# Kernel optimization log

Measured on AMD Instinct MI355X. Metric: run time of the kernel, lower is better.

The kernel has to match this reference:

```python
import jax, jax.numpy as jnp
import numpy as np

NUM_HEADS = 6
WS = 3

def setup_inputs() -> dict:
    key = jax.random.key(0)
    k1, k2, k3 = jax.random.split(key, 3)
    dim = 192
    x = jax.random.normal(k1, (2, dim, 48, 48, 48), dtype=jnp.float32)
    Wqkv = jax.random.normal(k2, (3 * dim, dim), dtype=jnp.float32) * (dim ** -0.5)
    Wproj = jax.random.normal(k3, (dim, dim), dtype=jnp.float32) * (dim ** -0.5)
    bproj = jnp.zeros((dim,), dtype=jnp.float32)
    return {"x": x, "Wqkv": Wqkv, "Wproj": Wproj, "bproj": bproj, "H": 384, "W": 288}

def reference(x, Wqkv, Wproj, bproj, H, W):
    b, c, h, w, d = x.shape
    xt = x.reshape(b, -1, c)                      # (B, N, C) with C = c, N = h*w*d
    B, N, C = xt.shape
    nh, ws = NUM_HEADS, WS
    hd = C // nh
    scale = hd ** -0.5
    hg, wg = H // ws, W // ws
    tg = hg * wg
    # window partition: (B, hg, ws, wg, ws, C) -> (B, hg, wg, ws, ws, C)
    xw = xt.reshape(B, hg, ws, wg, ws, C).transpose(0, 1, 3, 2, 4, 5)
    # fused QKV projection (no bias)
    qkv = jnp.einsum('bgvijc,oc->bgvijo', xw, Wqkv)          # (B,hg,wg,ws,ws,3C)
    qkv = qkv.reshape(B, tg, ws * ws, 3, nh, hd).transpose(3, 0, 1, 4, 2, 5)
    q, k, v = qkv[0], qkv[1], qkv[2]                          # (B, tg, nh, 9, hd)
    attn = jnp.einsum('bgnqd,bgnkd->bgnqk', q, k) * scale     # (B, tg, nh, 9, 9)
    attn = jax.nn.softmax(attn, axis=-1)
    out = jnp.einsum('bgnqk,bgnkd->bgnqd', attn, v)           # (B, tg, nh, 9, hd)
    out = out.transpose(0, 1, 3, 2, 4).reshape(B, hg, wg, ws, ws, C)
    out = jnp.swapaxes(out, 2, 3).reshape(B, N, C)            # un-window
    out = out @ Wproj.T + bproj
    return out.reshape(b, c, h, w, d)
```

## Files before the change

### kernel.cpp

```cpp
#include <hip/hip_runtime.h>

typedef _Float16 f16;
typedef _Float16 f16x4 __attribute__((ext_vector_type(4)));
typedef _Float16 f16x8 __attribute__((ext_vector_type(8)));
typedef float f32x4 __attribute__((ext_vector_type(4)));

#define TPB  576
#define NWIN 16
#define XS   200
#define WSS  200
#define QS   40
#define VS   260
#define VSF  264

#define WSQF_HALVES 110592
#define WS_NEEDED   (221184 + 73728)

__global__ __launch_bounds__(512) void conv_w(
    const float* __restrict__ Wqkv, const float* __restrict__ Wproj,
    f16* __restrict__ wsWqf, f16* __restrict__ wsWpf)
{
    int idx = blockIdx.x * 512 + threadIdx.x;
    if (idx < WSQF_HALVES) {
        int h    = idx / 18432;
        int rem  = idx % 18432;
        int ct   = rem / 3072;
        int rem2 = rem % 3072;
        int kk   = rem2 / 512;
        int rem3 = rem2 % 512;
        int lane = rem3 / 8;
        int e    = rem3 % 8;
        int r    = 16 * ct + (lane & 15);
        int grow = (r >> 5) * 192 + h * 32 + (r & 31);
        int col  = kk * 32 + (lane >> 4) * 8 + e;
        wsWqf[idx] = (f16)Wqkv[grow * 192 + col];
    } else {
        int j    = idx - WSQF_HALVES;
        int h    = j / 6144;
        int rem  = j % 6144;
        int nt   = rem / 512;
        int rem2 = rem % 512;
        int lane = rem2 / 8;
        int e    = rem2 % 8;
        wsWpf[j] = (f16)Wproj[(16 * nt + (lane & 15)) * 192 + h * 32 + (lane >> 4) * 8 + e];
    }
}

__global__ __launch_bounds__(TPB) void lsa_mfma12(
    const float* __restrict__ x, const f16* __restrict__ wsWqf,
    const f16* __restrict__ wsWpf, const float* __restrict__ bproj,
    float* __restrict__ out)
{
    __shared__ __attribute__((aligned(16))) f16 Xh[144 * XS];
    __shared__ __attribute__((aligned(16))) f16 Qh2[2][144 * QS];
    __shared__ __attribute__((aligned(16))) f16 Kh2[2][144 * QS];
    __shared__ __attribute__((aligned(16))) f16 Vt2[2][32 * VS];
    __shared__ __attribute__((aligned(16))) f16 AOh2[2][144 * QS];

    const int tid  = threadIdx.x;
    const int lane = tid & 63;
    const int w    = tid >> 6;
    const int ci   = w / 3;
    const int ti   = w % 3;
    const int l15  = lane & 15;
    const int lg   = lane >> 4;

    const int  bb    = blockIdx.x / 768;
    const int  gbase = (blockIdx.x % 768) * NWIN;
    const long rb0   = (long)bb * 110592 + (long)(gbase / 96) * 864 + (long)(gbase % 96) * 3;

    const f16x8* wqf = (const f16x8*)wsWqf;
    const f16x8* wpf = (const f16x8*)wsWpf;

    for (int idx = tid; idx < 144 * 48; idx += TPB) {
        int t = idx / 48, c4 = idx % 48;
        int wi = t / 9, q = t - 9 * wi;
        long grow = rb0 + wi * 3 + (q / 3) * 288 + (q % 3);
        float4 xv = ((const float4*)x)[grow * 48 + c4];
        union { f16 h[4]; ushort4 u; } tmp;
        tmp.h[0] = (f16)xv.x; tmp.h[1] = (f16)xv.y; tmp.h[2] = (f16)xv.z; tmp.h[3] = (f16)xv.w;
        *(ushort4*)&Xh[t * XS + c4 * 4] = tmp.u;
    }
    {
        int4 z = {0, 0, 0, 0};
        for (int i2 = tid; i2 < (2 * 32 * VS * 2) / 16; i2 += TPB) ((int4*)Vt2)[i2] = z;
    }

    f32x4 pacc[3][4];
    #pragma unroll
    for (int a = 0; a < 3; ++a)
        #pragma unroll
        for (int bq = 0; bq < 4; ++bq)
            pacc[a][bq] = (f32x4){0.f, 0.f, 0.f, 0.f};

    __syncthreads();

    for (int p = 0; p < 3; ++p) {
        #pragma unroll
        for (int hh = 0; hh < 2; ++hh) {
            const int h = 2 * p + hh;
            f32x4 qacc[2][3];
            #pragma unroll
            for (int c = 0; c < 2; ++c)
                #pragma unroll
                for (int t = 0; t < 3; ++t)
                    qacc[c][t] = (f32x4){0.f, 0.f, 0.f, 0.f};
            #pragma unroll
            for (int kk = 0; kk < 6; ++kk) {
                f16x8 af[2], bf[3];
                af[0] = wqf[((h * 6 + ci    ) * 6 + kk) * 64 + lane];
                af[1] = wqf[((h * 6 + ci + 3) * 6 + kk) * 64 + lane];
                #pragma unroll
                for (int t = 0; t < 3; ++t)
                    bf[t] = *(const f16x8*)&Xh[(16 * (ti + 3 * t) + l15) * XS + kk * 32 + lg * 8];
                #pragma unroll
                for (int c = 0; c < 2; ++c)
                    #pragma unroll
                    for (int t = 0; t < 3; ++t)
                        qacc[c][t] = __builtin_amdgcn_mfma_f32_16x16x32_f16(af[c], bf[t], qacc[c][t], 0, 0, 0);
            }
            #pragma unroll
            for (int c = 0; c < 2; ++c) {
                const int ct = ci + 3 * c;
                #pragma unroll
                for (int t = 0; t < 3; ++t) {
                    const int token = 16 * (ti + 3 * t) + l15;
                    f16x4 ph;
                    ph[0] = (f16)qacc[c][t][0]; ph[1] = (f16)qacc[c][t][1];
                    ph[2] = (f16)qacc[c][t][2]; ph[3] = (f16)qacc[c][t][3];
                    if (ct < 2) {
                        *(f16x4*)&Qh2[hh][token * QS + ct * 16 + 4 * lg] = ph;
                    } else if (ct < 4) {
                        *(f16x4*)&Kh2[hh][token * QS + (ct - 2) * 16 + 4 * lg] = ph;
                    } else {
                        const int d0 = (ct - 4) * 16 + 4 * lg;
                        int wi = token / 9, qq = token - 9 * wi;
                        #pragma unroll
                        for (int r = 0; r < 4; ++r)
                            Vt2[hh][(d0 + r) * VS + 16 * wi + qq] = ph[r];
                    }
                }
            }
        }
        __syncthreads();

        for (int idx = w; idx < 32; idx += 9) {
            const int hh = idx >> 4;
            const int wi = idx & 15;
            const f16* Qb = &Qh2[hh][0];
            const f16* Kb = &Kh2[hh][0];
            const f16* Vb = &Vt2[hh][0];
            f16* Ab = &AOh2[hh][0];
            int krow = 9 * wi + l15;
            krow = krow > 143 ? 143 : krow;
            f16x8 ak = *(const f16x8*)&Kb[krow * QS + lg * 8];
            f16x8 aq = *(const f16x8*)&Qb[krow * QS + lg * 8];
            f32x4 s = (f32x4){0.f, 0.f, 0.f, 0.f};
            s = __builtin_amdgcn_mfma_f32_16x16x32_f16(ak, aq, s, 0, 0, 0);
            float lgt[4];
            float mx = -1e30f;
            #pragma unroll
            for (int r = 0; r < 4; ++r) {
                int kx = 4 * lg + r;
                lgt[r] = (kx < 9) ? s[r] * 0.17677669529663687f : -1e30f;
                mx = fmaxf(mx, lgt[r]);
            }
            mx = fmaxf(mx, __shfl_xor(mx, 16));
            mx = fmaxf(mx, __shfl_xor(mx, 32));
            float e[4], sum = 0.f;
            #pragma unroll
            for (int r = 0; r < 4; ++r) {
                int kx = 4 * lg + r;
                e[r] = (kx < 9) ? __expf(lgt[r] - mx) : 0.f;
                sum += e[r];
            }
            sum += __shfl_xor(sum, 16);
            sum += __shfl_xor(sum, 32);
            float inv = 1.0f / sum;
            f16x4 pfrag;
            pfrag[0] = (f16)(e[0] * inv); pfrag[1] = (f16)(e[1] * inv);
            pfrag[2] = (f16)(e[2] * inv); pfrag[3] = (f16)(e[3] * inv);
            #pragma unroll
            for (int dt = 0; dt < 2; ++dt) {
                f16x4 av = *(const f16x4*)&Vb[(dt * 16 + l15) * VS + 16 * wi + 4 * lg];
                f32x4 o = (f32x4){0.f, 0.f, 0.f, 0.f};
                o = __builtin_amdgcn_mfma_f32_16x16x16f16(av, pfrag, o, 0, 0, 0);
                if (l15 < 9) {
                    f16x4 oh;
                    oh[0] = (f16)o[0]; oh[1] = (f16)o[1]; oh[2] = (f16)o[2]; oh[3] = (f16)o[3];
                    *(f16x4*)&Ab[(9 * wi + l15) * QS + dt * 16 + 4 * lg] = oh;
                }
            }
        }
        __syncthreads();

        #pragma unroll
        for (int hh = 0; hh < 2; ++hh) {
            const int h = 2 * p + hh;
            f16x8 bw[4];
            #pragma unroll
            for (int bq = 0; bq < 4; ++bq)
                bw[bq] = wpf[(h * 12 + 4 * ti + bq) * 64 + lane];
            f16x8 aof[3];
            #pragma unroll
            for (int a = 0; a < 3; ++a)
                aof[a] = *(const f16x8*)&AOh2[hh][(16 * (3 * ci + a) + l15) * QS + lg * 8];
            #pragma unroll
            for (int bq = 0; bq < 4; ++bq)
                #pragma unroll
                for (int a = 0; a < 3; ++a)
                    pacc[a][bq] = __builtin_amdgcn_mfma_f32_16x16x32_f16(aof[a], bw[bq], pacc[a][bq], 0, 0, 0);
        }
    }

    float bv[4];
    #pragma unroll
    for (int bq = 0; bq < 4; ++bq)
        bv[bq] = bproj[16 * (4 * ti + bq) + l15];
    #pragma unroll
    for (int a = 0; a < 3; ++a) {
        #pragma unroll
        for (int r = 0; r < 4; ++r) {
            int t = 16 * (3 * ci + a) + lg * 4 + r;
            int wi = t / 9, q = t - 9 * wi;
            long grow = rb0 + wi * 3 + (q / 3) * 288 + (q % 3);
            float* dst = out + grow * 192;
            #pragma unroll
            for (int bq = 0; bq < 4; ++bq)
                dst[16 * (4 * ti + bq) + l15] = pacc[a][bq][r] + bv[bq];
        }
    }
}

__global__ __launch_bounds__(TPB) void lsa_mfma7(
    const float* __restrict__ x, const float* __restrict__ Wqkv,
    const float* __restrict__ Wproj, const float* __restrict__ bproj,
    float* __restrict__ out)
{
    __shared__ f16 Xh[144 * XS];
    __shared__ f16 Wh[96 * WSS];
    __shared__ f16 Qh[144 * QS];
    __shared__ f16 Kh[144 * QS];
    __shared__ f16 Vt2f[32 * VSF];
    __shared__ f16 AOh[144 * QS];
    __shared__ f16 Wp[192 * QS];

    const int tid  = threadIdx.x;
    const int lane = tid & 63;
    const int w    = tid >> 6;
    const int ci   = w / 3;
    const int ti   = w % 3;
    const int l15  = lane & 15;
    const int lg   = lane >> 4;

    const int  bb    = blockIdx.x / 768;
    const int  gbase = (blockIdx.x % 768) * NWIN;
    const long rb0   = (long)bb * 110592 + (long)(gbase / 96) * 864 + (long)(gbase % 96) * 3;

    const float4* Wq4 = (const float4*)Wqkv;
    const float4* Wp4 = (const float4*)Wproj;

    for (int idx = tid; idx < 144 * 48; idx += TPB) {
        int t = idx / 48, c4 = idx % 48;
        int wi = t / 9, q = t - 9 * wi;
        long grow = rb0 + wi * 3 + (q / 3) * 288 + (q % 3);
        float4 xv = ((const float4*)x)[grow * 48 + c4];
        union { f16 h[4]; ushort4 u; } tmp;
        tmp.h[0] = (f16)xv.x; tmp.h[1] = (f16)xv.y; tmp.h[2] = (f16)xv.z; tmp.h[3] = (f16)xv.w;
        *(ushort4*)&Xh[t * XS + c4 * 4] = tmp.u;
    }
    {
        int4 z = {0, 0, 0, 0};
        for (int i2 = tid; i2 < (32 * VSF * 2) / 16; i2 += TPB) ((int4*)Vt2f)[i2] = z;
    }
    #pragma unroll
    for (int i = 0; i < 8; ++i) {
        int l = i * TPB + tid;
        int r = l / 48, c4 = l % 48;
        float4 wv = Wq4[((r >> 5) * 192 + (r & 31)) * 48 + c4];
        union { f16 h4[4]; ushort4 u; } t;
        t.h4[0] = (f16)wv.x; t.h4[1] = (f16)wv.y; t.h4[2] = (f16)wv.z; t.h4[3] = (f16)wv.w;
        *(ushort4*)&Wh[r * WSS + c4 * 4] = t.u;
    }

    f32x4 pacc[3][4];
    #pragma unroll
    for (int a = 0; a < 3; ++a)
        #pragma unroll
        for (int bq = 0; bq < 4; ++bq)
            pacc[a][bq] = (f32x4){0.f, 0.f, 0.f, 0.f};

    __syncthreads();

    for (int h = 0; h < 6; ++h) {
        f32x4 qacc[2][3];
        #pragma unroll
        for (int c = 0; c < 2; ++c)
            #pragma unroll
            for (int t = 0; t < 3; ++t)
                qacc[c][t] = (f32x4){0.f, 0.f, 0.f, 0.f};
        #pragma unroll
        for (int kk = 0; kk < 6; ++kk) {
            f16x8 af[2], bf[3];
            #pragma unroll
            for (int c = 0; c < 2; ++c)
                af[c] = *(const f16x8*)&Wh[(16 * (ci + 3 * c) + l15) * WSS + kk * 32 + lg * 8];
            #pragma unroll
            for (int t = 0; t < 3; ++t)
                bf[t] = *(const f16x8*)&Xh[(16 * (ti + 3 * t) + l15) * XS + kk * 32 + lg * 8];
            #pragma unroll
            for (int c = 0; c < 2; ++c)
                #pragma unroll
                for (int t = 0; t < 3; ++t)
                    qacc[c][t] = __builtin_amdgcn_mfma_f32_16x16x32_f16(af[c], bf[t], qacc[c][t], 0, 0, 0);
        }
        #pragma unroll
        for (int c = 0; c < 2; ++c) {
            const int ct = ci + 3 * c;
            #pragma unroll
            for (int t = 0; t < 3; ++t) {
                const int token = 16 * (ti + 3 * t) + l15;
                f16x4 ph;
                ph[0] = (f16)qacc[c][t][0]; ph[1] = (f16)qacc[c][t][1];
                ph[2] = (f16)qacc[c][t][2]; ph[3] = (f16)qacc[c][t][3];
                if (ct < 2) {
                    *(f16x4*)&Qh[token * QS + ct * 16 + 4 * lg] = ph;
                } else if (ct < 4) {
                    *(f16x4*)&Kh[token * QS + (ct - 2) * 16 + 4 * lg] = ph;
                } else {
                    const int d0 = (ct - 4) * 16 + 4 * lg;
                    int wi = token / 9, qq = token - 9 * wi;
                    #pragma unroll
                    for (int r = 0; r < 4; ++r)
                        Vt2f[(d0 + r) * VSF + 16 * wi + qq] = ph[r];
                }
            }
        }
        __syncthreads();

        float4 wpv[3];
        if (tid < 512) {
            #pragma unroll
            for (int i = 0; i < 3; ++i) {
                int l = i * 512 + tid;
                int r = l / 8, c4 = l % 8;
                wpv[i] = Wp4[r * 48 + h * 8 + c4];
            }
        }
        if (h < 5) {
            #pragma unroll
            for (int i = 0; i < 8; ++i) {
                int l = i * TPB + tid;
                int r = l / 48, c4 = l % 48;
                float4 wv = Wq4[((r >> 5) * 192 + (h + 1) * 32 + (r & 31)) * 48 + c4];
                union { f16 h4[4]; ushort4 u; } t;
                t.h4[0] = (f16)wv.x; t.h4[1] = (f16)wv.y; t.h4[2] = (f16)wv.z; t.h4[3] = (f16)wv.w;
                *(ushort4*)&Wh[r * WSS + c4 * 4] = t.u;
            }
        }
        for (int wi = w; wi < NWIN; wi += 9) {
            int krow = 9 * wi + l15;
            krow = krow > 143 ? 143 : krow;
            f16x8 ak = *(const f16x8*)&Kh[krow * QS + lg * 8];
            f16x8 aq = *(const f16x8*)&Qh[krow * QS + lg * 8];
            f32x4 s = (f32x4){0.f, 0.f, 0.f, 0.f};
            s = __builtin_amdgcn_mfma_f32_16x16x32_f16(ak, aq, s, 0, 0, 0);
            float lgt[4];
            float mx = -1e30f;
            #pragma unroll
            for (int r = 0; r < 4; ++r) {
                int kx = 4 * lg + r;
                lgt[r] = (kx < 9) ? s[r] * 0.17677669529663687f : -1e30f;
                mx = fmaxf(mx, lgt[r]);
            }
            mx = fmaxf(mx, __shfl_xor(mx, 16));
            mx = fmaxf(mx, __shfl_xor(mx, 32));
            float e[4], sum = 0.f;
            #pragma unroll
            for (int r = 0; r < 4; ++r) {
                int kx = 4 * lg + r;
                e[r] = (kx < 9) ? __expf(lgt[r] - mx) : 0.f;
                sum += e[r];
            }
            sum += __shfl_xor(sum, 16);
            sum += __shfl_xor(sum, 32);
            float inv = 1.0f / sum;
            f16x4 pf;
            pf[0] = (f16)(e[0] * inv); pf[1] = (f16)(e[1] * inv);
            pf[2] = (f16)(e[2] * inv); pf[3] = (f16)(e[3] * inv);
            #pragma unroll
            for (int dt = 0; dt < 2; ++dt) {
                f16x4 av = *(const f16x4*)&Vt2f[(dt * 16 + l15) * VSF + 16 * wi + 4 * lg];
                f32x4 o = (f32x4){0.f, 0.f, 0.f, 0.f};
                o = __builtin_amdgcn_mfma_f32_16x16x16f16(av, pf, o, 0, 0, 0);
                if (l15 < 9) {
                    f16x4 oh;
                    oh[0] = (f16)o[0]; oh[1] = (f16)o[1]; oh[2] = (f16)o[2]; oh[3] = (f16)o[3];
                    *(f16x4*)&AOh[(9 * wi + l15) * QS + dt * 16 + 4 * lg] = oh;
                }
            }
        }
        if (tid < 512) {
            #pragma unroll
            for (int i = 0; i < 3; ++i) {
                int l = i * 512 + tid;
                int r = l / 8, c4 = l % 8;
                union { f16 h4[4]; ushort4 u; } t;
                t.h4[0] = (f16)wpv[i].x; t.h4[1] = (f16)wpv[i].y;
                t.h4[2] = (f16)wpv[i].z; t.h4[3] = (f16)wpv[i].w;
                *(ushort4*)&Wp[r * QS + c4 * 4] = t.u;
            }
        }
        __syncthreads();

        {
            f16x8 aof[3];
            #pragma unroll
            for (int a = 0; a < 3; ++a)
                aof[a] = *(const f16x8*)&AOh[(16 * (3 * ci + a) + l15) * QS + lg * 8];
            #pragma unroll
            for (int bq = 0; bq < 4; ++bq) {
                f16x8 bw = *(const f16x8*)&Wp[(16 * (4 * ti + bq) + l15) * QS + lg * 8];
                #pragma unroll
                for (int a = 0; a < 3; ++a)
                    pacc[a][bq] = __builtin_amdgcn_mfma_f32_16x16x32_f16(aof[a], bw, pacc[a][bq], 0, 0, 0);
            }
        }
    }

    float bv[4];
    #pragma unroll
    for (int bq = 0; bq < 4; ++bq)
        bv[bq] = bproj[16 * (4 * ti + bq) + l15];
    #pragma unroll
    for (int a = 0; a < 3; ++a) {
        #pragma unroll
        for (int r = 0; r < 4; ++r) {
            int t = 16 * (3 * ci + a) + lg * 4 + r;
            int wi = t / 9, q = t - 9 * wi;
            long grow = rb0 + wi * 3 + (q / 3) * 288 + (q % 3);
            float* dst = out + grow * 192;
            #pragma unroll
            for (int bq = 0; bq < 4; ++bq)
                dst[16 * (4 * ti + bq) + l15] = pacc[a][bq][r] + bv[bq];
        }
    }
}

extern "C" void kernel_launch(void* const* d_in, const int* in_sizes, int n_in,
                              void* d_out, int out_size, void* d_ws, size_t ws_size,
                              hipStream_t stream) {
    const float* x     = (const float*)d_in[0];
    const float* Wqkv  = (const float*)d_in[1];
    const float* Wproj = (const float*)d_in[2];
    const float* bproj = (const float*)d_in[3];
    float* out = (float*)d_out;
    if (ws_size >= (size_t)WS_NEEDED && d_ws != nullptr) {
        f16* wsWqf = (f16*)d_ws;
        f16* wsWpf = (f16*)((char*)d_ws + 221184);
        conv_w<<<288, 512, 0, stream>>>(Wqkv, Wproj, wsWqf, wsWpf);
        lsa_mfma12<<<1536, TPB, 0, stream>>>(x, wsWqf, wsWpf, bproj, out);
    } else {
        lsa_mfma7<<<1536, TPB, 0, stream>>>(x, Wqkv, Wproj, bproj, out);
    }
}
```

Measured before the change: 221.8 us.

## Software-pipeline QKV, attention and projection across heads with one barrier per head

Replaces the two-heads-per-pass loop with a three-stage software pipeline. In each head iteration it computes QKV for the next head, attention for the current head and the output projection for the previous head, using double-buffered shared memory and a single barrier per iteration. The aim is to overlap the poorly balanced attention phase (16 windows spread over 9 waves) with MFMA-heavy GEMM work and to shorten the serial phase chain. The risks are higher register pressure from mixing all three stages in one loop, and one more barrier overall.

```diff
diff --git a/kernel.cpp b/kernel.cpp
--- a/kernel.cpp
+++ b/kernel.cpp
@@ -46,7 +46,7 @@
     }
 }
 
-__global__ __launch_bounds__(TPB) void lsa_mfma12(
+__global__ __launch_bounds__(TPB) void lsa_mfma13(
     const float* __restrict__ x, const f16* __restrict__ wsWqf,
     const f16* __restrict__ wsWpf, const float* __restrict__ bproj,
     float* __restrict__ out)
@@ -93,64 +93,57 @@
         for (int bq = 0; bq < 4; ++bq)
             pacc[a][bq] = (f32x4){0.f, 0.f, 0.f, 0.f};
 
-    __syncthreads();
-
-    for (int p = 0; p < 3; ++p) {
-        #pragma unroll
-        for (int hh = 0; hh < 2; ++hh) {
-            const int h = 2 * p + hh;
-            f32x4 qacc[2][3];
+    auto qkv_head = [&](int h, int hb) {
+        f32x4 qacc[2][3];
+        #pragma unroll
+        for (int c = 0; c < 2; ++c)
+            #pragma unroll
+            for (int t = 0; t < 3; ++t)
+                qacc[c][t] = (f32x4){0.f, 0.f, 0.f, 0.f};
+        #pragma unroll
+        for (int kk = 0; kk < 6; ++kk) {
+            f16x8 af[2], bf[3];
+            af[0] = wqf[((h * 6 + ci    ) * 6 + kk) * 64 + lane];
+            af[1] = wqf[((h * 6 + ci + 3) * 6 + kk) * 64 + lane];
+            #pragma unroll
+            for (int t = 0; t < 3; ++t)
+                bf[t] = *(const f16x8*)&Xh[(16 * (ti + 3 * t) + l15) * XS + kk * 32 + lg * 8];
             #pragma unroll
             for (int c = 0; c < 2; ++c)
                 #pragma unroll
                 for (int t = 0; t < 3; ++t)
-                    qacc[c][t] = (f32x4){0.f, 0.f, 0.f, 0.f};
-            #pragma unroll
-            for (int kk = 0; kk < 6; ++kk) {
-                f16x8 af[2], bf[3];
-                af[0] = wqf[((h * 6 + ci    ) * 6 + kk) * 64 + lane];
-                af[1] = wqf[((h * 6 + ci + 3) * 6 + kk) * 64 + lane];
-                #pragma unroll
-                for (int t = 0; t < 3; ++t)
-                    bf[t] = *(const f16x8*)&Xh[(16 * (ti + 3 * t) + l15) * XS + kk * 32 + lg * 8];
-                #pragma unroll
-                for (int c = 0; c < 2; ++c)
+                    qacc[c][t] = __builtin_amdgcn_mfma_f32_16x16x32_f16(af[c], bf[t], qacc[c][t], 0, 0, 0);
+        }
+        #pragma unroll
+        for (int c = 0; c < 2; ++c) {
+            const int ct = ci + 3 * c;
+            #pragma unroll
+            for (int t = 0; t < 3; ++t) {
+                const int token = 16 * (ti + 3 * t) + l15;
+                f16x4 ph;
+                ph[0] = (f16)qacc[c][t][0]; ph[1] = (f16)qacc[c][t][1];
+                ph[2] = (f16)qacc[c][t][2]; ph[3] = (f16)qacc[c][t][3];
+                if (ct < 2) {
+                    *(f16x4*)&Qh2[hb][token * QS + ct * 16 + 4 * lg] = ph;
+                } else if (ct < 4) {
+                    *(f16x4*)&Kh2[hb][token * QS + (ct - 2) * 16 + 4 * lg] = ph;
+                } else {
+                    const int d0 = (ct - 4) * 16 + 4 * lg;
+                    int wi = token / 9, qq = token - 9 * wi;
                     #pragma unroll
-                    for (int t = 0; t < 3; ++t)
-                        qacc[c][t] = __builtin_amdgcn_mfma_f32_16x16x32_f16(af[c], bf[t], qacc[c][t], 0, 0, 0);
-            }
-            #pragma unroll
-            for (int c = 0; c < 2; ++c) {
-                const int ct = ci + 3 * c;
-                #pragma unroll
-                for (int t = 0; t < 3; ++t) {
-                    const int token = 16 * (ti + 3 * t) + l15;
-                    f16x4 ph;
-                    ph[0] = (f16)qacc[c][t][0]; ph[1] = (f16)qacc[c][t][1];
-                    ph[2] = (f16)qacc[c][t][2]; ph[3] = (f16)qacc[c][t][3];
-                    if (ct < 2) {
-                        *(f16x4*)&Qh2[hh][token * QS + ct * 16 + 4 * lg] = ph;
-                    } else if (ct < 4) {
-                        *(f16x4*)&Kh2[hh][token * QS + (ct - 2) * 16 + 4 * lg] = ph;
-                    } else {
-                        const int d0 = (ct - 4) * 16 + 4 * lg;
-                        int wi = token / 9, qq = token - 9 * wi;
-                        #pragma unroll
-                        for (int r = 0; r < 4; ++r)
-                            Vt2[hh][(d0 + r) * VS + 16 * wi + qq] = ph[r];
-                    }
+                    for (int r = 0; r < 4; ++r)
+                        Vt2[hb][(d0 + r) * VS + 16 * wi + qq] = ph[r];
                 }
             }
         }
-        __syncthreads();
-
-        for (int idx = w; idx < 32; idx += 9) {
-            const int hh = idx >> 4;
-            const int wi = idx & 15;
-            const f16* Qb = &Qh2[hh][0];
-            const f16* Kb = &Kh2[hh][0];
-            const f16* Vb = &Vt2[hh][0];
-            f16* Ab = &AOh2[hh][0];
+    };
+
+    auto attn_head = [&](int hb) {
+        const f16* Qb = &Qh2[hb][0];
+        const f16* Kb = &Kh2[hb][0];
+        const f16* Vb = &Vt2[hb][0];
+        f16* Ab = &AOh2[hb][0];
+        for (int wi = w; wi < NWIN; wi += 9) {
             int krow = 9 * wi + l15;
             krow = krow > 143 ? 143 : krow;
             f16x8 ak = *(const f16x8*)&Kb[krow * QS + lg * 8];
@@ -192,26 +185,37 @@
                 }
             }
         }
+    };
+
+    auto proj_head = [&](int h, int hb) {
+        f16x8 bw[4];
+        #pragma unroll
+        for (int bq = 0; bq < 4; ++bq)
+            bw[bq] = wpf[(h * 12 + 4 * ti + bq) * 64 + lane];
+        f16x8 aof[3];
+        #pragma unroll
+        for (int a = 0; a < 3; ++a)
+            aof[a] = *(const f16x8*)&AOh2[hb][(16 * (3 * ci + a) + l15) * QS + lg * 8];
+        #pragma unroll
+        for (int bq = 0; bq < 4; ++bq)
+            #pragma unroll
+            for (int a = 0; a < 3; ++a)
+                pacc[a][bq] = __builtin_amdgcn_mfma_f32_16x16x32_f16(aof[a], bw[bq], pacc[a][bq], 0, 0, 0);
+    };
+
+    __syncthreads();
+
+    qkv_head(0, 0);
+    __syncthreads();
+
+    for (int h = 0; h < 6; ++h) {
+        const int cur = h & 1;
+        if (h < 5) qkv_head(h + 1, cur ^ 1);
+        attn_head(cur);
+        if (h > 0) proj_head(h - 1, cur ^ 1);
         __syncthreads();
-
-        #pragma unroll
-        for (int hh = 0; hh < 2; ++hh) {
-            const int h = 2 * p + hh;
-            f16x8 bw[4];
-            #pragma unroll
-            for (int bq = 0; bq < 4; ++bq)
-                bw[bq] = wpf[(h * 12 + 4 * ti + bq) * 64 + lane];
-            f16x8 aof[3];
-            #pragma unroll
-            for (int a = 0; a < 3; ++a)
-                aof[a] = *(const f16x8*)&AOh2[hh][(16 * (3 * ci + a) + l15) * QS + lg * 8];
-            #pragma unroll
-            for (int bq = 0; bq < 4; ++bq)
-                #pragma unroll
-                for (int a = 0; a < 3; ++a)
-                    pacc[a][bq] = __builtin_amdgcn_mfma_f32_16x16x32_f16(aof[a], bw[bq], pacc[a][bq], 0, 0, 0);
-        }
-    }
+    }
+    proj_head(5, 1);
 
     float bv[4];
     #pragma unroll
@@ -459,7 +463,7 @@
         f16* wsWqf = (f16*)d_ws;
         f16* wsWpf = (f16*)((char*)d_ws + 221184);
         conv_w<<<288, 512, 0, stream>>>(Wqkv, Wproj, wsWqf, wsWpf);
-        lsa_mfma12<<<1536, TPB, 0, stream>>>(x, wsWqf, wsWpf, bproj, out);
+        lsa_mfma13<<<1536, TPB, 0, stream>>>(x, wsWqf, wsWpf, bproj, out);
     } else {
         lsa_mfma7<<<1536, TPB, 0, stream>>>(x, Wqkv, Wproj, bproj, out);
     }
```

After: 217.5 us. No clear change (-1.9%).
